# Optimization experiments

Hardware: AMD Instinct MI355X
Metric: run time of the kernel (lower is better)

## Reference

```python
import jax, jax.numpy as jnp
import numpy as np

ND, NP_, NC, H, L, B = 4000, 19000, 1000, 128, 2, 30000
E_DP, E_PP, E_CP = 200000, 300000, 150000


def setup_inputs() -> dict:
    key = jax.random.key(0)
    ks = iter(jax.random.split(key, 64))
    def nrm(shape, s=0.05):
        return jax.random.normal(next(ks), shape, dtype=jnp.float32) * s
    inp = {
        'drug_emb': nrm((ND, H)), 'protein_emb': nrm((NP_, H)), 'cell_emb': nrm((NC, H)),
    }
    for r in ['dp', 'rdp', 'pp', 'cp', 'rcp']:
        inp['W_' + r] = nrm((L, H, H))
        inp['a_src_' + r] = nrm((L, H))
        inp['a_dst_' + r] = nrm((L, H))
        inp['b_' + r] = jnp.zeros((L, H), jnp.float32)
    inp['W1'] = nrm((3 * H, 6 * H)); inp['b1'] = jnp.zeros((6 * H,), jnp.float32)
    inp['W2'] = nrm((6 * H, 2 * H)); inp['b2'] = jnp.zeros((2 * H,), jnp.float32)
    inp['W3'] = nrm((2 * H, 2)); inp['b3'] = jnp.zeros((2,), jnp.float32)
    def ri(n, hi):
        return jax.random.randint(next(ks), (n,), 0, hi, dtype=jnp.int32)
    inp['src_dp'] = ri(E_DP, ND); inp['dst_dp'] = ri(E_DP, NP_)
    inp['src_pp'] = ri(E_PP, NP_); inp['dst_pp'] = ri(E_PP, NP_)
    inp['src_cp'] = ri(E_CP, NC); inp['dst_cp'] = ri(E_CP, NP_)
    inp['drug1'] = ri(B, ND); inp['drug2'] = ri(B, ND); inp['cell'] = ri(B, NC)
    return inp


def _gat(x_src, x_dst, W, a_s, a_d, b, src, dst, n_dst):
    # Single-head PyG GATConv: shared linear, additive attention, segment softmax over dst.
    h_s = x_src @ W                      # [Ns, H]
    h_d = x_dst @ W                      # [Nd, H]
    e = jax.nn.leaky_relu((h_s @ a_s)[src] + (h_d @ a_d)[dst], 0.2)  # [E]
    m = jax.lax.stop_gradient(jax.ops.segment_max(e, dst, num_segments=n_dst))
    p = jnp.exp(e - m[dst])
    denom = jax.ops.segment_sum(p, dst, num_segments=n_dst)
    alpha = p / denom[dst]
    out = jax.ops.segment_sum(alpha[:, None] * h_s[src], dst, num_segments=n_dst)
    return out + b


def _l2norm(x):
    return x / jnp.maximum(jnp.linalg.norm(x, axis=1, keepdims=True), 1e-12)


def reference(drug_emb, protein_emb, cell_emb,
              W_dp, a_src_dp, a_dst_dp, b_dp,
              W_rdp, a_src_rdp, a_dst_rdp, b_rdp,
              W_pp, a_src_pp, a_dst_pp, b_pp,
              W_cp, a_src_cp, a_dst_cp, b_cp,
              W_rcp, a_src_rcp, a_dst_rcp, b_rcp,
              W1, b1, W2, b2, W3, b3,
              src_dp, dst_dp, src_pp, dst_pp, src_cp, dst_cp,
              drug1, drug2, cell):
    # p-p uses add_self_loops=True
    loops = jnp.arange(NP_, dtype=src_pp.dtype)
    spp = jnp.concatenate([src_pp, loops]); dpp = jnp.concatenate([dst_pp, loops])
    x_d, x_p, x_c = drug_emb, protein_emb, cell_emb
    for l in range(L):
        out_p = _gat(x_d, x_p, W_dp[l], a_src_dp[l], a_dst_dp[l], b_dp[l], src_dp, dst_dp, NP_)
        out_p = out_p + _gat(x_p, x_p, W_pp[l], a_src_pp[l], a_dst_pp[l], b_pp[l], spp, dpp, NP_)
        out_p = out_p + _gat(x_c, x_p, W_cp[l], a_src_cp[l], a_dst_cp[l], b_cp[l], src_cp, dst_cp, NP_)
        out_d = _gat(x_p, x_d, W_rdp[l], a_src_rdp[l], a_dst_rdp[l], b_rdp[l], dst_dp, src_dp, ND)
        out_c = _gat(x_p, x_c, W_rcp[l], a_src_rcp[l], a_dst_rcp[l], b_rcp[l], dst_cp, src_cp, NC)
        x_d, x_p, x_c = jax.nn.relu(out_d), jax.nn.relu(out_p), jax.nn.relu(out_c)
    hid = jnp.concatenate([_l2norm(x_d[drug1]), _l2norm(x_d[drug2]), _l2norm(x_c[cell])], axis=1)
    h = jax.nn.relu(hid @ W1 + b1)
    h = jax.nn.relu(h @ W2 + b2)
    return h @ W3 + b3
```

## Files before the change

### kernel.cpp

```cpp
#include <hip/hip_runtime.h>
#include <hip/hip_bf16.h>

#define H 128
#define ND 4000
#define NPN 19000
#define NCN 1000
#define NLAYERS 2
#define NB 30000
#define E_DP 200000
#define E_PP 300000
#define E_CP 150000

typedef __bf16 bf16_t;
typedef bf16_t bf16x8 __attribute__((ext_vector_type(8)));
typedef float f32x4 __attribute__((ext_vector_type(4)));
typedef unsigned short u16;

static __device__ __forceinline__ float wred_sum(float v) {
#pragma unroll
  for (int off = 32; off; off >>= 1) v += __shfl_xor(v, off);
  return v;
}
static __device__ __forceinline__ float bflo(unsigned u) { return __uint_as_float(u << 16); }
static __device__ __forceinline__ float bfhi(unsigned u) { return __uint_as_float(u & 0xffff0000u); }
static __device__ __forceinline__ unsigned packbf(float v0, float v1) {
  union { bf16_t b; unsigned short u; } a, b;
  a.b = (bf16_t)v0; b.b = (bf16_t)v1;
  return (unsigned)a.u | ((unsigned)b.u << 16);
}

#define GLDS16(gp, lp) \
  __builtin_amdgcn_global_load_lds((__attribute__((address_space(1))) void*)(gp), \
                                   (__attribute__((address_space(3))) void*)(lp), 16, 0, 0)

__device__ __forceinline__ void mfma_core(
    const bf16_t* __restrict__ A, const bf16_t* __restrict__ Bt,
    int M, int K, int ldb, int m0, int n0, f32x4 (&acc)[4][4])
{
  __shared__ char As[128 * 64];
  __shared__ char Bs[128 * 64];
  const int t = threadIdx.x;
  const int lane = t & 63;
#pragma unroll
  for (int mi = 0; mi < 4; ++mi)
#pragma unroll
    for (int ni = 0; ni < 4; ++ni) acc[mi][ni] = (f32x4){0.f, 0.f, 0.f, 0.f};

  const int wid = t >> 6;
  const int wr = wid >> 1, wc = wid & 1;
  const int sr = t >> 2;
  const int sc = t & 3;
  const int csrc = ((sc ^ ((sr >> 1) & 3)) << 4);
  int ra0 = m0 + sr;      if (ra0 >= M) ra0 = M - 1;
  int ra1 = m0 + 64 + sr; if (ra1 >= M) ra1 = M - 1;
  const char* gA0 = (const char*)A + (size_t)ra0 * K * 2 + csrc;
  const char* gA1 = (const char*)A + (size_t)ra1 * K * 2 + csrc;
  const char* gB0 = (const char*)Bt + (size_t)(n0 + sr) * ldb * 2 + csrc;
  const char* gB1 = (const char*)Bt + (size_t)(n0 + 64 + sr) * ldb * 2 + csrc;
  char* lA0 = As + t * 16;
  char* lA1 = As + 4096 + t * 16;
  char* lB0 = Bs + t * 16;
  char* lB1 = Bs + 4096 + t * 16;

  int aoff[4], boff[4];
#pragma unroll
  for (int mi = 0; mi < 4; ++mi) {
    int r = wr * 64 + mi * 16 + (lane & 15);
    aoff[mi] = r * 64 + ((((lane >> 4)) ^ ((r >> 1) & 3)) << 4);
  }
#pragma unroll
  for (int ni = 0; ni < 4; ++ni) {
    int r = wc * 64 + ni * 16 + (lane & 15);
    boff[ni] = r * 64 + ((((lane >> 4)) ^ ((r >> 1) & 3)) << 4);
  }

  for (int k0 = 0; k0 < K; k0 += 32) {
    const size_t kb = (size_t)k0 * 2;
    __syncthreads();
    GLDS16(gA0 + kb, lA0);
    GLDS16(gA1 + kb, lA1);
    GLDS16(gB0 + kb, lB0);
    GLDS16(gB1 + kb, lB1);
    __syncthreads();
    bf16x8 av[4], bv[4];
#pragma unroll
    for (int mi = 0; mi < 4; ++mi) av[mi] = *(const bf16x8*)(As + aoff[mi]);
#pragma unroll
    for (int ni = 0; ni < 4; ++ni) bv[ni] = *(const bf16x8*)(Bs + boff[ni]);
#pragma unroll
    for (int mi = 0; mi < 4; ++mi)
#pragma unroll
      for (int ni = 0; ni < 4; ++ni)
        acc[mi][ni] = __builtin_amdgcn_mfma_f32_16x16x32_bf16(av[mi], bv[ni], acc[mi][ni], 0, 0, 0);
  }
}

struct GJob { const bf16_t* A; const bf16_t* Bt; bf16_t* C; int M; int K;
              const float *b1, *b2, *b3; };
struct Gemm3 { GJob j[3]; };
__global__ __launch_bounds__(256) void k_gemm_g3(Gemm3 g) {
  const GJob& jb = g.j[blockIdx.y];
  int m0 = blockIdx.x * 128;
  if (m0 >= jb.M) return;
  f32x4 acc[4][4];
  mfma_core(jb.A, jb.Bt, jb.M, jb.K, jb.K, m0, 0, acc);
  const int t = threadIdx.x, lane = t & 63, wid = t >> 6;
  const int wr = wid >> 1, wc = wid & 1;
  const int col0 = lane & 15, rsub = (lane >> 4) * 4;
#pragma unroll
  for (int mi = 0; mi < 4; ++mi) {
#pragma unroll
    for (int ni = 0; ni < 4; ++ni) {
      int c = wc * 64 + ni * 16 + col0;
      float bb = jb.b1[c];
      if (jb.b2) bb += jb.b2[c];
      if (jb.b3) bb += jb.b3[c];
#pragma unroll
      for (int rg = 0; rg < 4; ++rg) {
        int r = m0 + wr * 64 + mi * 16 + rsub + rg;
        if (r < jb.M) jb.C[(size_t)r * H + c] = (bf16_t)fmaxf(acc[mi][ni][rg] + bb, 0.f);
      }
    }
  }
}

struct PJob { const bf16_t* A; float* C; int M; const float* rs; };
struct GemmPS { PJob j[3]; const bf16_t* Bt; };
__global__ __launch_bounds__(256) void k_gemm_ps(GemmPS g) {
  const PJob& jb = g.j[blockIdx.y];
  int mt = blockIdx.x / 6, nt = blockIdx.x - mt * 6;
  int m0 = mt * 128;
  if (m0 >= jb.M) return;
  int n0 = nt * 128;
  f32x4 acc[4][4];
  mfma_core(jb.A, g.Bt + blockIdx.y * 128, jb.M, 128, 384, m0, n0, acc);
  const int t = threadIdx.x, lane = t & 63, wid = t >> 6;
  const int wr = wid >> 1, wc = wid & 1;
  const int col0 = lane & 15, rsub = (lane >> 4) * 4;
#pragma unroll
  for (int mi = 0; mi < 4; ++mi) {
#pragma unroll
    for (int rg = 0; rg < 4; ++rg) {
      int r = m0 + wr * 64 + mi * 16 + rsub + rg;
      if (r < jb.M) {
        float sc = jb.rs[r];
#pragma unroll
        for (int ni = 0; ni < 4; ++ni) {
          int c = n0 + wc * 64 + ni * 16 + col0;
          jb.C[(size_t)r * 768 + c] = acc[mi][ni][rg] * sc;
        }
      }
    }
  }
}

__global__ __launch_bounds__(256) void k_w2head(
    const float* __restrict__ Pa, const float* __restrict__ Pb, const float* __restrict__ Pc,
    const float* __restrict__ b1,
    const int* __restrict__ d1, const int* __restrict__ d2, const int* __restrict__ ce,
    const bf16_t* __restrict__ W2t, const float* __restrict__ b2,
    const float* __restrict__ W3, const float* __restrict__ b3,
    float* __restrict__ out, int cn)
{
  __shared__ char As[128 * 64];
  __shared__ char Bs[128 * 64];
  const int t = threadIdx.x;
  const int lane = t & 63;
  const int m0 = blockIdx.x * 128;
  const int n0 = blockIdx.y * 128;
  if (m0 >= cn) return;
  f32x4 acc[4][4];
#pragma unroll
  for (int mi = 0; mi < 4; ++mi)
#pragma unroll
    for (int ni = 0; ni < 4; ++ni) acc[mi][ni] = (f32x4){0.f, 0.f, 0.f, 0.f};

  const int arow = t >> 1;
  const int ah = t & 1;
  int gr = m0 + arow; if (gr >= cn) gr = cn - 1;
  const float* pa = Pa + (size_t)d1[gr] * 768 + ah * 16;
  const float* pb = Pb + (size_t)d2[gr] * 768 + ah * 16;
  const float* pc = Pc + (size_t)ce[gr] * 768 + ah * 16;
  const int swz = (arow >> 1) & 3;
  char* la0 = As + arow * 64 + (((ah * 2)     ^ swz) << 4);
  char* la1 = As + arow * 64 + (((ah * 2 + 1) ^ swz) << 4);

  const int sr = t >> 2;
  const int sc = t & 3;
  const int csrc = ((sc ^ ((sr >> 1) & 3)) << 4);
  const char* gB0 = (const char*)W2t + (size_t)(n0 + sr) * 768 * 2 + csrc;
  const char* gB1 = (const char*)W2t + (size_t)(n0 + 64 + sr) * 768 * 2 + csrc;
  char* lB0 = Bs + t * 16;
  char* lB1 = Bs + 4096 + t * 16;

  const int wid = t >> 6;
  const int wr = wid >> 1, wc = wid & 1;
  int aoff[4], boff[4];
#pragma unroll
  for (int mi = 0; mi < 4; ++mi) {
    int r = wr * 64 + mi * 16 + (lane & 15);
    aoff[mi] = r * 64 + ((((lane >> 4)) ^ ((r >> 1) & 3)) << 4);
  }
#pragma unroll
  for (int ni = 0; ni < 4; ++ni) {
    int r = wc * 64 + ni * 16 + (lane & 15);
    boff[ni] = r * 64 + ((((lane >> 4)) ^ ((r >> 1) & 3)) << 4);
  }

  for (int k0 = 0; k0 < 768; k0 += 32) {
    const float4* qa = (const float4*)(pa + k0);
    const float4* qb = (const float4*)(pb + k0);
    const float4* qc = (const float4*)(pc + k0);
    const float4* qb1 = (const float4*)(b1 + k0 + ah * 16);
    float4 A0 = qa[0], A1 = qa[1], A2 = qa[2], A3 = qa[3];
    float4 B0 = qb[0], B1 = qb[1], B2 = qb[2], B3 = qb[3];
    float4 C0 = qc[0], C1 = qc[1], C2 = qc[2], C3 = qc[3];
    float4 D0 = qb1[0], D1 = qb1[1], D2 = qb1[2], D3 = qb1[3];
    uint4 P0, P1;
    P0.x = packbf(fmaxf(A0.x + B0.x + C0.x + D0.x, 0.f), fmaxf(A0.y + B0.y + C0.y + D0.y, 0.f));
    P0.y = packbf(fmaxf(A0.z + B0.z + C0.z + D0.z, 0.f), fmaxf(A0.w + B0.w + C0.w + D0.w, 0.f));
    P0.z = packbf(fmaxf(A1.x + B1.x + C1.x + D1.x, 0.f), fmaxf(A1.y + B1.y + C1.y + D1.y, 0.f));
    P0.w = packbf(fmaxf(A1.z + B1.z + C1.z + D1.z, 0.f), fmaxf(A1.w + B1.w + C1.w + D1.w, 0.f));
    P1.x = packbf(fmaxf(A2.x + B2.x + C2.x + D2.x, 0.f), fmaxf(A2.y + B2.y + C2.y + D2.y, 0.f));
    P1.y = packbf(fmaxf(A2.z + B2.z + C2.z + D2.z, 0.f), fmaxf(A2.w + B2.w + C2.w + D2.w, 0.f));
    P1.z = packbf(fmaxf(A3.x + B3.x + C3.x + D3.x, 0.f), fmaxf(A3.y + B3.y + C3.y + D3.y, 0.f));
    P1.w = packbf(fmaxf(A3.z + B3.z + C3.z + D3.z, 0.f), fmaxf(A3.w + B3.w + C3.w + D3.w, 0.f));
    __syncthreads();
    GLDS16(gB0 + (size_t)k0 * 2, lB0);
    GLDS16(gB1 + (size_t)k0 * 2, lB1);
    *(uint4*)la0 = P0;
    *(uint4*)la1 = P1;
    __syncthreads();
    bf16x8 av[4], bv[4];
#pragma unroll
    for (int mi = 0; mi < 4; ++mi) av[mi] = *(const bf16x8*)(As + aoff[mi]);
#pragma unroll
    for (int ni = 0; ni < 4; ++ni) bv[ni] = *(const bf16x8*)(Bs + boff[ni]);
#pragma unroll
    for (int mi = 0; mi < 4; ++mi)
#pragma unroll
      for (int ni = 0; ni < 4; ++ni)
        acc[mi][ni] = __builtin_amdgcn_mfma_f32_16x16x32_bf16(av[mi], bv[ni], acc[mi][ni], 0, 0, 0);
  }

  const int col0 = lane & 15, rsub = (lane >> 4) * 4;
  float w0[4], w1[4], bb[4];
#pragma unroll
  for (int ni = 0; ni < 4; ++ni) {
    int c = n0 + wc * 64 + ni * 16 + col0;
    w0[ni] = W3[2 * c]; w1[ni] = W3[2 * c + 1]; bb[ni] = b2[c];
  }
  const int addb = (n0 == 0 && wc == 0);
#pragma unroll
  for (int mi = 0; mi < 4; ++mi) {
#pragma unroll
    for (int rg = 0; rg < 4; ++rg) {
      int r = m0 + wr * 64 + mi * 16 + rsub + rg;
      float p0 = 0.f, p1 = 0.f;
#pragma unroll
      for (int ni = 0; ni < 4; ++ni) {
        float v = fmaxf(acc[mi][ni][rg] + bb[ni], 0.f);
        p0 = fmaf(v, w0[ni], p0);
        p1 = fmaf(v, w1[ni], p1);
      }
#pragma unroll
      for (int off = 1; off < 16; off <<= 1) {
        p0 += __shfl_xor(p0, off);
        p1 += __shfl_xor(p1, off);
      }
      if (col0 == 0 && r < cn) {
        if (addb) { p0 += b3[0]; p1 += b3[1]; }
        atomicAdd(&out[(size_t)r * 2], p0);
        atomicAdd(&out[(size_t)r * 2 + 1], p1);
      }
    }
  }
}

__global__ __launch_bounds__(256) void k_conv_emb(
    const float* __restrict__ xd, const float* __restrict__ xp, const float* __restrict__ xc,
    bf16_t* __restrict__ od, bf16_t* __restrict__ op, bf16_t* __restrict__ oc)
{
  int i = blockIdx.x * 256 + threadIdx.x;
  const int SD = ND * H, SP = NPN * H, SC = NCN * H;
  if (i < SD) od[i] = (bf16_t)xd[i];
  else if (i < SD + SP) op[i - SD] = (bf16_t)xp[i - SD];
  else if (i < SD + SP + SC) oc[i - SD - SP] = (bf16_t)xc[i - SD - SP];
}

struct TC { const float* src[12]; bf16_t* dst[12]; int Ksub[12]; int N[12]; int Kfull[12]; int koff[12]; };
__global__ __launch_bounds__(256) void k_tconv2(TC a) {
  int m = blockIdx.z;
  int Ks = a.Ksub[m], N = a.N[m];
  int tx = blockIdx.x * 32;
  int ty = blockIdx.y * 32;
  if (tx >= N || ty >= Ks) return;
  __shared__ float tile[32][33];
  int c = threadIdx.x & 31, rr = threadIdx.x >> 5;
#pragma unroll
  for (int kk = rr; kk < 32; kk += 8)
    if (ty + kk < Ks && tx + c < N) tile[kk][c] = a.src[m][(size_t)(ty + kk) * N + tx + c];
  __syncthreads();
  bf16_t* dst = a.dst[m];
  int Kf = a.Kfull[m], ko = a.koff[m];
#pragma unroll
  for (int nn = rr; nn < 32; nn += 8)
    if (tx + nn < N && ty + c < Ks)
      dst[(size_t)(tx + nn) * Kf + ko + ty + c] = (bf16_t)tile[c][nn];
}

struct Wd20 { const float* W[20]; const float* a[20]; float* o[20]; };
__global__ __launch_bounds__(128) void k_wd20(Wd20 g) {
  int m = blockIdx.x;
  int k = threadIdx.x;
  const float* Wp = g.W[m];
  const float* av = g.a[m];
  float s = 0.f;
#pragma unroll 4
  for (int j = 0; j < H; ++j) s = fmaf(Wp[k * H + j], av[j], s);
  g.o[m][k] = s;
}

struct Sc { const bf16_t* xd; const bf16_t* xp; const bf16_t* xc; const float* wv;
            float* ss[5]; float* sd[5]; };
__global__ __launch_bounds__(256) void k_scores(Sc S) {
  int row = blockIdx.x * 4 + (threadIdx.x >> 6);
  if (row >= ND + NPN + NCN) return;
  int lane = threadIdx.x & 63;
  const bf16_t* x;
  int idx, cls;
  if (row < ND) { x = S.xd; idx = row; cls = 0; }
  else if (row < ND + NPN) { x = S.xp; idx = row - ND; cls = 1; }
  else { x = S.xc; idx = row - ND - NPN; cls = 2; }
  unsigned u = *(const unsigned*)(x + (size_t)idx * H + lane * 2);
  float x0 = bflo(u), x1 = bfhi(u);
  const float* wv = S.wv;
#define DOT(vi, outp) { const float* v = wv + (vi) * H; \
    float s = x0 * v[2 * lane] + x1 * v[2 * lane + 1]; s = wred_sum(s); \
    if (!lane) (outp)[idx] = s; }
  if (cls == 0) {
    DOT(0, S.ss[0]); DOT(8, S.sd[3]);
  } else if (cls == 1) {
    DOT(1, S.ss[1]); DOT(3, S.ss[3]); DOT(4, S.ss[4]);
    DOT(5, S.sd[0]); DOT(6, S.sd[1]); DOT(7, S.sd[2]);
  } else {
    DOT(2, S.ss[2]); DOT(9, S.sd[4]);
  }
#undef DOT
}

struct CsrArgs {
  const int* src[5]; const int* dst[5];
  int E[5]; int n[5];
  int* cnt[5]; int* cur[5]; int* starts[5]; u16* csr[5];
};
__global__ __launch_bounds__(256) void k_count5(CsrArgs a) {
  int rel = blockIdx.y;
  int E = a.E[rel];
  const int* dst = a.dst[rel];
  int* cnt = a.cnt[rel];
  int e0 = blockIdx.x * 1024 + threadIdx.x;
#pragma unroll
  for (int u = 0; u < 4; ++u) {
    int e = e0 + u * 256;
    if (e < E) atomicAdd(&cnt[dst[e]], 1);
  }
}
__global__ __launch_bounds__(1024) void k_scan5(CsrArgs a) {
  int rel = blockIdx.x;
  int n = a.n[rel];
  const int* cnt = a.cnt[rel];
  int* st = a.starts[rel];
  int* cu = a.cur[rel];
  int t = threadIdx.x;
  int stripe = (n + 1023) / 1024;
  int lo = t * stripe;
  int hi = lo + stripe; if (hi > n) hi = n;
  int s = 0;
  for (int i = lo; i < hi; ++i) s += cnt[i];
  int lane = t & 63, wv = t >> 6;
  int x = s;
#pragma unroll
  for (int off = 1; off < 64; off <<= 1) {
    int y = __shfl_up(x, off);
    if (lane >= off) x += y;
  }
  __shared__ int ws[16];
  if (lane == 63) ws[wv] = x;
  __syncthreads();
  if (t == 0) {
    int run = 0;
#pragma unroll
    for (int i = 0; i < 16; ++i) { int v = ws[i]; ws[i] = run; run += v; }
  }
  __syncthreads();
  int run = ws[wv] + x - s;
  for (int i = lo; i < hi; ++i) { st[i] = run; cu[i] = run; run += cnt[i]; }
  if (t == 1023) st[n] = ws[15] + x;
}
__global__ __launch_bounds__(256) void k_fill5(CsrArgs a) {
  int rel = blockIdx.y;
  int E = a.E[rel];
  const int* dst = a.dst[rel];
  const int* src = a.src[rel];
  int* cur = a.cur[rel];
  u16* csr = a.csr[rel];
  int e0 = blockIdx.x * 1024 + threadIdx.x;
#pragma unroll
  for (int u = 0; u < 4; ++u) {
    int e = e0 + u * 256;
    if (e < E) {
      int pos = atomicAdd(&cur[dst[e]], 1);
      csr[pos] = (u16)src[e];
    }
  }
}

struct Agg5 {
  const u16* csr[5]; const int* starts[5];
  const float* ss[5]; const float* sd[5];
  const bf16_t* xs[5];
  bf16_t* y[5]; int ystride[5]; int ycoff[5]; int ndst[5]; int self[5];
};
__global__ __launch_bounds__(256) void k_agg5(Agg5 a) {
  int rel = blockIdx.y;
  int d = blockIdx.x * 4 + (threadIdx.x >> 6);
  if (d >= a.ndst[rel]) return;
  int lane = threadIdx.x & 63;
  int g = lane >> 4, j16 = lane & 15;
  bf16_t* yrow = a.y[rel] + (size_t)d * a.ystride[rel] + a.ycoff[rel];
  int s0 = a.starts[rel][d];
  int deg = a.starts[rel][d + 1] - s0;
  int selfa = a.self[rel];
  if (!deg && !selfa) {
    if (g == 0) *(uint4*)(yrow + j16 * 8) = make_uint4(0u, 0u, 0u, 0u);
    return;
  }
  const u16* cs = a.csr[rel] + s0;
  const float* ssp = a.ss[rel];
  const bf16_t* xsp = a.xs[rel];
  float sdv = a.sd[rel][d];
  float acc[8] = {0.f, 0.f, 0.f, 0.f, 0.f, 0.f, 0.f, 0.f};
  float ps = 0.f;
  for (int b = 0; b < deg; b += 16) {
#pragma unroll
    for (int u = 0; u < 4; ++u) {
      int i = b + u * 4 + g;
      float p = 0.f;
      uint4 U = make_uint4(0u, 0u, 0u, 0u);
      if (i < deg) {
        int s = cs[i];
        float e = ssp[s] + sdv; e = e > 0.f ? e : 0.2f * e;
        p = __expf(e);
        U = *(const uint4*)(xsp + (size_t)s * H + j16 * 8);
      }
      ps += p;
      acc[0] = fmaf(p, bflo(U.x), acc[0]); acc[1] = fmaf(p, bfhi(U.x), acc[1]);
      acc[2] = fmaf(p, bflo(U.y), acc[2]); acc[3] = fmaf(p, bfhi(U.y), acc[3]);
      acc[4] = fmaf(p, bflo(U.z), acc[4]); acc[5] = fmaf(p, bfhi(U.z), acc[5]);
      acc[6] = fmaf(p, bflo(U.w), acc[6]); acc[7] = fmaf(p, bfhi(U.w), acc[7]);
    }
  }
  if (selfa && g == 0) {
    float e = ssp[d] + sdv; e = e > 0.f ? e : 0.2f * e;
    float p = __expf(e);
    uint4 U = *(const uint4*)(xsp + (size_t)d * H + j16 * 8);
    ps += p;
    acc[0] = fmaf(p, bflo(U.x), acc[0]); acc[1] = fmaf(p, bfhi(U.x), acc[1]);
    acc[2] = fmaf(p, bflo(U.y), acc[2]); acc[3] = fmaf(p, bfhi(U.y), acc[3]);
    acc[4] = fmaf(p, bflo(U.z), acc[4]); acc[5] = fmaf(p, bfhi(U.z), acc[5]);
    acc[6] = fmaf(p, bflo(U.w), acc[6]); acc[7] = fmaf(p, bfhi(U.w), acc[7]);
  }
#pragma unroll
  for (int e = 0; e < 8; ++e) {
    acc[e] += __shfl_xor(acc[e], 16);
    acc[e] += __shfl_xor(acc[e], 32);
  }
  ps += __shfl_xor(ps, 16);
  ps += __shfl_xor(ps, 32);
  if (g == 0) {
    float inv = 1.f / ps;
    uint4 O;
    O.x = packbf(acc[0] * inv, acc[1] * inv);
    O.y = packbf(acc[2] * inv, acc[3] * inv);
    O.z = packbf(acc[4] * inv, acc[5] * inv);
    O.w = packbf(acc[6] * inv, acc[7] * inv);
    *(uint4*)(yrow + j16 * 8) = O;
  }
}

__global__ __launch_bounds__(256) void k_invnorm(
    const bf16_t* __restrict__ xd, const bf16_t* __restrict__ xc,
    float* __restrict__ invd, float* __restrict__ invc)
{
  int row = blockIdx.x * 4 + (threadIdx.x >> 6);
  if (row >= ND + NCN) return;
  int lane = threadIdx.x & 63;
  const bf16_t* x = (row < ND) ? xd + (size_t)row * H : xc + (size_t)(row - ND) * H;
  unsigned u = ((const unsigned*)x)[lane];
  float av = bflo(u), bv = bfhi(u);
  float s = wred_sum(av * av + bv * bv);
  if (!lane) {
    float nv = fmaxf(sqrtf(s), 1e-12f);
    if (row < ND) invd[row] = 1.f / nv; else invc[row - ND] = 1.f / nv;
  }
}

extern "C" void kernel_launch(void* const* d_in, const int* in_sizes, int n_in,
                              void* d_out, int out_size, void* d_ws, size_t ws_size,
                              hipStream_t stream)
{
  (void)in_sizes; (void)n_in;
  const float* drug_emb    = (const float*)d_in[0];
  const float* protein_emb = (const float*)d_in[1];
  const float* cell_emb    = (const float*)d_in[2];
  const int base_idx[5] = {3, 11, 15, 7, 19};
  const float *W_[5], *as_[5], *ad_[5], *b_[5];
  for (int r = 0; r < 5; ++r) {
    W_[r]  = (const float*)d_in[base_idx[r]];
    as_[r] = (const float*)d_in[base_idx[r] + 1];
    ad_[r] = (const float*)d_in[base_idx[r] + 2];
    b_[r]  = (const float*)d_in[base_idx[r] + 3];
  }
  const float* W1 = (const float*)d_in[23]; const float* b1 = (const float*)d_in[24];
  const float* W2 = (const float*)d_in[25]; const float* b2 = (const float*)d_in[26];
  const float* W3 = (const float*)d_in[27]; const float* b3 = (const float*)d_in[28];
  const int* src_dp = (const int*)d_in[29]; const int* dst_dp = (const int*)d_in[30];
  const int* src_pp = (const int*)d_in[31]; const int* dst_pp = (const int*)d_in[32];
  const int* src_cp = (const int*)d_in[33]; const int* dst_cp = (const int*)d_in[34];
  const int* drug1  = (const int*)d_in[35]; const int* drug2  = (const int*)d_in[36];
  const int* cellb  = (const int*)d_in[37];
  float* out = (float*)d_out;

  char* wsb = (char*)d_ws;
  size_t off = 0;
  auto alloc = [&](size_t bytes) -> void* {
    void* p = wsb + off;
    off += (bytes + 255) & ~(size_t)255;
    return p;
  };
  bf16_t* xdb[2] = {(bf16_t*)alloc((size_t)ND * H * 2),  (bf16_t*)alloc((size_t)ND * H * 2)};
  bf16_t* xpb[2] = {(bf16_t*)alloc((size_t)NPN * H * 2), (bf16_t*)alloc((size_t)NPN * H * 2)};
  bf16_t* xcb[2] = {(bf16_t*)alloc((size_t)NCN * H * 2), (bf16_t*)alloc((size_t)NCN * H * 2)};
  const int Msrc[5] = {ND, NPN, NCN, NPN, NPN};
  const int Mdst[5] = {NPN, NPN, NPN, ND, NCN};
  const int Erel[5] = {E_DP, E_PP, E_CP, E_DP, E_CP};
  bf16_t* yp = (bf16_t*)alloc((size_t)NPN * 384 * 2);
  bf16_t* yd = (bf16_t*)alloc((size_t)ND * H * 2);
  bf16_t* yc = (bf16_t*)alloc((size_t)NCN * H * 2);
  bf16_t* Wtp = (bf16_t*)alloc((size_t)NLAYERS * 128 * 384 * 2);
  bf16_t* Wtd = (bf16_t*)alloc((size_t)NLAYERS * 128 * 128 * 2);
  bf16_t* Wtc = (bf16_t*)alloc((size_t)NLAYERS * 128 * 128 * 2);
  bf16_t* W1t = (bf16_t*)alloc((size_t)768 * 384 * 2);
  bf16_t* W2t = (bf16_t*)alloc((size_t)256 * 768 * 2);
  float* wvb = (float*)alloc(20 * H * 4);
  float* ssb[5]; for (int r = 0; r < 5; ++r) ssb[r] = (float*)alloc((size_t)Msrc[r] * 4);
  float* sdb[5]; for (int r = 0; r < 5; ++r) sdb[r] = (float*)alloc((size_t)Mdst[r] * 4);
  int* cnt_all = (int*)alloc(62000 * 4);
  int* cur_all = (int*)alloc(62000 * 4);
  int* st_all  = (int*)alloc((62000 + 5) * 4);
  int *cntb[5], *curb[5], *stb[5];
  { int o = 0, o2 = 0;
    for (int r = 0; r < 5; ++r) {
      cntb[r] = cnt_all + o; curb[r] = cur_all + o; stb[r] = st_all + o2;
      o += Mdst[r]; o2 += Mdst[r] + 1;
    } }
  u16* csrb[5]; for (int r = 0; r < 5; ++r) csrb[r] = (u16*)alloc((size_t)Erel[r] * 2);
  float* invd = (float*)alloc(ND * 4);
  float* invc = (float*)alloc(NCN * 4);
  float* P1a = (float*)alloc((size_t)ND * 768 * 4);
  float* P1b = (float*)alloc((size_t)ND * 768 * 4);
  float* P1c = (float*)alloc((size_t)NCN * 768 * 4);
  (void)ws_size;

  hipMemsetAsync(out, 0, (size_t)out_size * 4, stream);

  k_conv_emb<<<(ND * H + NPN * H + NCN * H + 255) / 256, 256, 0, stream>>>(
      drug_emb, protein_emb, cell_emb, xdb[0], xpb[0], xcb[0]);
  TC tc;
  for (int l = 0; l < 2; ++l) {
    for (int r = 0; r < 3; ++r) {
      int m = l * 3 + r;
      tc.src[m] = W_[r] + (size_t)l * H * H;
      tc.dst[m] = Wtp + (size_t)l * 128 * 384;
      tc.Ksub[m] = 128; tc.N[m] = 128; tc.Kfull[m] = 384; tc.koff[m] = r * 128;
    }
    tc.src[6 + l] = W_[3] + (size_t)l * H * H; tc.dst[6 + l] = Wtd + (size_t)l * 128 * 128;
    tc.Ksub[6 + l] = 128; tc.N[6 + l] = 128; tc.Kfull[6 + l] = 128; tc.koff[6 + l] = 0;
    tc.src[8 + l] = W_[4] + (size_t)l * H * H; tc.dst[8 + l] = Wtc + (size_t)l * 128 * 128;
    tc.Ksub[8 + l] = 128; tc.N[8 + l] = 128; tc.Kfull[8 + l] = 128; tc.koff[8 + l] = 0;
  }
  tc.src[10] = W1; tc.dst[10] = W1t; tc.Ksub[10] = 384; tc.N[10] = 768; tc.Kfull[10] = 384; tc.koff[10] = 0;
  tc.src[11] = W2; tc.dst[11] = W2t; tc.Ksub[11] = 768; tc.N[11] = 256; tc.Kfull[11] = 768; tc.koff[11] = 0;
  k_tconv2<<<dim3(24, 24, 12), 256, 0, stream>>>(tc);

  Wd20 wg;
  for (int l = 0; l < 2; ++l)
    for (int r = 0; r < 5; ++r) {
      int m = l * 10 + r;
      wg.W[m] = W_[r] + (size_t)l * H * H; wg.a[m] = as_[r] + l * H; wg.o[m] = wvb + m * H;
      int m2 = l * 10 + 5 + r;
      wg.W[m2] = W_[r] + (size_t)l * H * H; wg.a[m2] = ad_[r] + l * H; wg.o[m2] = wvb + m2 * H;
    }
  k_wd20<<<20, 128, 0, stream>>>(wg);

  hipMemsetAsync(cnt_all, 0, 62000 * 4, stream);
  CsrArgs ca;
  const int* srcA[5] = {src_dp, src_pp, src_cp, dst_dp, dst_cp};
  const int* dstA[5] = {dst_dp, dst_pp, dst_cp, src_dp, src_cp};
  for (int r = 0; r < 5; ++r) {
    ca.src[r] = srcA[r]; ca.dst[r] = dstA[r]; ca.E[r] = Erel[r]; ca.n[r] = Mdst[r];
    ca.cnt[r] = cntb[r]; ca.cur[r] = curb[r]; ca.starts[r] = stb[r]; ca.csr[r] = csrb[r];
  }
  dim3 egrid((E_PP + 1023) / 1024, 5);
  k_count5<<<egrid, 256, 0, stream>>>(ca);
  k_scan5<<<5, 1024, 0, stream>>>(ca);
  k_fill5<<<egrid, 256, 0, stream>>>(ca);

  int cur = 0;
  for (int l = 0; l < NLAYERS; ++l) {
    int nxt = 1 - cur;
    const bf16_t* xsrc[5] = {xdb[cur], xpb[cur], xcb[cur], xpb[cur], xpb[cur]};
    Sc sc;
    sc.xd = xdb[cur]; sc.xp = xpb[cur]; sc.xc = xcb[cur]; sc.wv = wvb + l * 10 * H;
    for (int r = 0; r < 5; ++r) { sc.ss[r] = ssb[r]; sc.sd[r] = sdb[r]; }
    k_scores<<<(ND + NPN + NCN + 3) / 4, 256, 0, stream>>>(sc);
    Agg5 aa;
    bf16_t* yptr[5] = {yp, yp, yp, yd, yc};
    const int ystr[5] = {384, 384, 384, 128, 128};
    const int ycof[5] = {0, 128, 256, 0, 0};
    const int selfs[5] = {0, 1, 0, 0, 0};
    for (int r = 0; r < 5; ++r) {
      aa.csr[r] = csrb[r]; aa.starts[r] = stb[r]; aa.ss[r] = ssb[r]; aa.sd[r] = sdb[r];
      aa.xs[r] = xsrc[r]; aa.y[r] = yptr[r]; aa.ystride[r] = ystr[r]; aa.ycoff[r] = ycof[r];
      aa.ndst[r] = Mdst[r]; aa.self[r] = selfs[r];
    }
    k_agg5<<<dim3((NPN + 3) / 4, 5), 256, 0, stream>>>(aa);
    Gemm3 g3;
    g3.j[0] = {yp, Wtp + (size_t)l * 128 * 384, xpb[nxt], NPN, 384,
               b_[0] + l * H, b_[1] + l * H, b_[2] + l * H};
    g3.j[1] = {yd, Wtd + (size_t)l * 128 * 128, xdb[nxt], ND, 128,
               b_[3] + l * H, nullptr, nullptr};
    g3.j[2] = {yc, Wtc + (size_t)l * 128 * 128, xcb[nxt], NCN, 128,
               b_[4] + l * H, nullptr, nullptr};
    k_gemm_g3<<<dim3((NPN + 127) / 128, 3), 256, 0, stream>>>(g3);
    cur = nxt;
  }

  k_invnorm<<<(ND + NCN + 3) / 4, 256, 0, stream>>>(xdb[cur], xcb[cur], invd, invc);
  GemmPS ps;
  ps.Bt = W1t;
  ps.j[0] = {xdb[cur], P1a, ND, invd};
  ps.j[1] = {xdb[cur], P1b, ND, invd};
  ps.j[2] = {xcb[cur], P1c, NCN, invc};
  k_gemm_ps<<<dim3(32 * 6, 3), 256, 0, stream>>>(ps);
  k_w2head<<<dim3((NB + 127) / 128, 2), 256, 0, stream>>>(
      P1a, P1b, P1c, b1, drug1, drug2, cellb, W2t, b2, W3, b3, out, NB);
}
```

Before: 418.3 us.

## Store W1 partial products in bf16, fold bias, widen head tile to full N

The per-table W1 partial products now go to bf16 instead of fp32, with a third of b1 folded into each partial so the head kernel no longer reads b1. The head kernel now covers all 256 output columns in one block instead of splitting N over two blocks. This halves the gathered bytes and avoids gathering each row twice. In exchange it doubles accumulator registers per thread, which may lower occupancy, and adds extra bf16 rounding in the partial sums.

```diff
diff --git a/kernel.cpp b/kernel.cpp
--- a/kernel.cpp
+++ b/kernel.cpp
@@ -124,8 +124,8 @@
   }
 }
 
-struct PJob { const bf16_t* A; float* C; int M; const float* rs; };
-struct GemmPS { PJob j[3]; const bf16_t* Bt; };
+struct PJob { const bf16_t* A; bf16_t* C; int M; const float* rs; };
+struct GemmPS { PJob j[3]; const bf16_t* Bt; const float* b1t; };
 __global__ __launch_bounds__(256) void k_gemm_ps(GemmPS g) {
   const PJob& jb = g.j[blockIdx.y];
   int mt = blockIdx.x / 6, nt = blockIdx.x - mt * 6;
@@ -147,7 +147,7 @@
 #pragma unroll
         for (int ni = 0; ni < 4; ++ni) {
           int c = n0 + wc * 64 + ni * 16 + col0;
-          jb.C[(size_t)r * 768 + c] = acc[mi][ni][rg] * sc;
+          jb.C[(size_t)r * 768 + c] = (bf16_t)(acc[mi][ni][rg] * sc + g.b1t[c]);
         }
       }
     }
@@ -155,32 +155,30 @@
 }
 
 __global__ __launch_bounds__(256) void k_w2head(
-    const float* __restrict__ Pa, const float* __restrict__ Pb, const float* __restrict__ Pc,
-    const float* __restrict__ b1,
+    const bf16_t* __restrict__ Pa, const bf16_t* __restrict__ Pb, const bf16_t* __restrict__ Pc,
     const int* __restrict__ d1, const int* __restrict__ d2, const int* __restrict__ ce,
     const bf16_t* __restrict__ W2t, const float* __restrict__ b2,
     const float* __restrict__ W3, const float* __restrict__ b3,
     float* __restrict__ out, int cn)
 {
   __shared__ char As[128 * 64];
-  __shared__ char Bs[128 * 64];
+  __shared__ char Bs[256 * 64];
   const int t = threadIdx.x;
   const int lane = t & 63;
   const int m0 = blockIdx.x * 128;
-  const int n0 = blockIdx.y * 128;
   if (m0 >= cn) return;
-  f32x4 acc[4][4];
+  f32x4 acc[4][8];
 #pragma unroll
   for (int mi = 0; mi < 4; ++mi)
 #pragma unroll
-    for (int ni = 0; ni < 4; ++ni) acc[mi][ni] = (f32x4){0.f, 0.f, 0.f, 0.f};
+    for (int ni = 0; ni < 8; ++ni) acc[mi][ni] = (f32x4){0.f, 0.f, 0.f, 0.f};
 
   const int arow = t >> 1;
   const int ah = t & 1;
   int gr = m0 + arow; if (gr >= cn) gr = cn - 1;
-  const float* pa = Pa + (size_t)d1[gr] * 768 + ah * 16;
-  const float* pb = Pb + (size_t)d2[gr] * 768 + ah * 16;
-  const float* pc = Pc + (size_t)ce[gr] * 768 + ah * 16;
+  const bf16_t* pa = Pa + (size_t)d1[gr] * 768 + ah * 16;
+  const bf16_t* pb = Pb + (size_t)d2[gr] * 768 + ah * 16;
+  const bf16_t* pc = Pc + (size_t)ce[gr] * 768 + ah * 16;
   const int swz = (arow >> 1) & 3;
   char* la0 = As + arow * 64 + (((ah * 2)     ^ swz) << 4);
   char* la1 = As + arow * 64 + (((ah * 2 + 1) ^ swz) << 4);
@@ -188,69 +186,75 @@
   const int sr = t >> 2;
   const int sc = t & 3;
   const int csrc = ((sc ^ ((sr >> 1) & 3)) << 4);
-  const char* gB0 = (const char*)W2t + (size_t)(n0 + sr) * 768 * 2 + csrc;
-  const char* gB1 = (const char*)W2t + (size_t)(n0 + 64 + sr) * 768 * 2 + csrc;
-  char* lB0 = Bs + t * 16;
-  char* lB1 = Bs + 4096 + t * 16;
+  const char* gB = (const char*)W2t + (size_t)sr * 768 * 2 + csrc;
+  const size_t qstep = (size_t)64 * 768 * 2;
 
   const int wid = t >> 6;
   const int wr = wid >> 1, wc = wid & 1;
-  int aoff[4], boff[4];
+  int aoff[4], boff[8];
 #pragma unroll
   for (int mi = 0; mi < 4; ++mi) {
     int r = wr * 64 + mi * 16 + (lane & 15);
     aoff[mi] = r * 64 + ((((lane >> 4)) ^ ((r >> 1) & 3)) << 4);
   }
 #pragma unroll
-  for (int ni = 0; ni < 4; ++ni) {
-    int r = wc * 64 + ni * 16 + (lane & 15);
+  for (int ni = 0; ni < 8; ++ni) {
+    int r = wc * 128 + ni * 16 + (lane & 15);
     boff[ni] = r * 64 + ((((lane >> 4)) ^ ((r >> 1) & 3)) << 4);
   }
 
+#define ACC8(U, o) { s[o+0] += bflo(U.x); s[o+1] += bfhi(U.x); s[o+2] += bflo(U.y); s[o+3] += bfhi(U.y); \
+                     s[o+4] += bflo(U.z); s[o+5] += bfhi(U.z); s[o+6] += bflo(U.w); s[o+7] += bfhi(U.w); }
   for (int k0 = 0; k0 < 768; k0 += 32) {
-    const float4* qa = (const float4*)(pa + k0);
-    const float4* qb = (const float4*)(pb + k0);
-    const float4* qc = (const float4*)(pc + k0);
-    const float4* qb1 = (const float4*)(b1 + k0 + ah * 16);
-    float4 A0 = qa[0], A1 = qa[1], A2 = qa[2], A3 = qa[3];
-    float4 B0 = qb[0], B1 = qb[1], B2 = qb[2], B3 = qb[3];
-    float4 C0 = qc[0], C1 = qc[1], C2 = qc[2], C3 = qc[3];
-    float4 D0 = qb1[0], D1 = qb1[1], D2 = qb1[2], D3 = qb1[3];
+    uint4 Ua0 = *(const uint4*)(pa + k0);
+    uint4 Ua1 = *(const uint4*)(pa + k0 + 8);
+    uint4 Ub0 = *(const uint4*)(pb + k0);
+    uint4 Ub1 = *(const uint4*)(pb + k0 + 8);
+    uint4 Uc0 = *(const uint4*)(pc + k0);
+    uint4 Uc1 = *(const uint4*)(pc + k0 + 8);
+    float s[16] = {0.f, 0.f, 0.f, 0.f, 0.f, 0.f, 0.f, 0.f,
+                   0.f, 0.f, 0.f, 0.f, 0.f, 0.f, 0.f, 0.f};
+    ACC8(Ua0, 0) ACC8(Ua1, 8)
+    ACC8(Ub0, 0) ACC8(Ub1, 8)
+    ACC8(Uc0, 0) ACC8(Uc1, 8)
     uint4 P0, P1;
-    P0.x = packbf(fmaxf(A0.x + B0.x + C0.x + D0.x, 0.f), fmaxf(A0.y + B0.y + C0.y + D0.y, 0.f));
-    P0.y = packbf(fmaxf(A0.z + B0.z + C0.z + D0.z, 0.f), fmaxf(A0.w + B0.w + C0.w + D0.w, 0.f));
-    P0.z = packbf(fmaxf(A1.x + B1.x + C1.x + D1.x, 0.f), fmaxf(A1.y + B1.y + C1.y + D1.y, 0.f));
-    P0.w = packbf(fmaxf(A1.z + B1.z + C1.z + D1.z, 0.f), fmaxf(A1.w + B1.w + C1.w + D1.w, 0.f));
-    P1.x = packbf(fmaxf(A2.x + B2.x + C2.x + D2.x, 0.f), fmaxf(A2.y + B2.y + C2.y + D2.y, 0.f));
-    P1.y = packbf(fmaxf(A2.z + B2.z + C2.z + D2.z, 0.f), fmaxf(A2.w + B2.w + C2.w + D2.w, 0.f));
-    P1.z = packbf(fmaxf(A3.x + B3.x + C3.x + D3.x, 0.f), fmaxf(A3.y + B3.y + C3.y + D3.y, 0.f));
-    P1.w = packbf(fmaxf(A3.z + B3.z + C3.z + D3.z, 0.f), fmaxf(A3.w + B3.w + C3.w + D3.w, 0.f));
+    P0.x = packbf(fmaxf(s[0], 0.f),  fmaxf(s[1], 0.f));
+    P0.y = packbf(fmaxf(s[2], 0.f),  fmaxf(s[3], 0.f));
+    P0.z = packbf(fmaxf(s[4], 0.f),  fmaxf(s[5], 0.f));
+    P0.w = packbf(fmaxf(s[6], 0.f),  fmaxf(s[7], 0.f));
+    P1.x = packbf(fmaxf(s[8], 0.f),  fmaxf(s[9], 0.f));
+    P1.y = packbf(fmaxf(s[10], 0.f), fmaxf(s[11], 0.f));
+    P1.z = packbf(fmaxf(s[12], 0.f), fmaxf(s[13], 0.f));
+    P1.w = packbf(fmaxf(s[14], 0.f), fmaxf(s[15], 0.f));
+    const size_t kb = (size_t)k0 * 2;
     __syncthreads();
-    GLDS16(gB0 + (size_t)k0 * 2, lB0);
-    GLDS16(gB1 + (size_t)k0 * 2, lB1);
+    GLDS16(gB + kb,             Bs + t * 16);
+    GLDS16(gB + qstep + kb,     Bs + 4096 + t * 16);
+    GLDS16(gB + 2 * qstep + kb, Bs + 8192 + t * 16);
+    GLDS16(gB + 3 * qstep + kb, Bs + 12288 + t * 16);
     *(uint4*)la0 = P0;
     *(uint4*)la1 = P1;
     __syncthreads();
-    bf16x8 av[4], bv[4];
+    bf16x8 av[4], bv[8];
 #pragma unroll
     for (int mi = 0; mi < 4; ++mi) av[mi] = *(const bf16x8*)(As + aoff[mi]);
 #pragma unroll
-    for (int ni = 0; ni < 4; ++ni) bv[ni] = *(const bf16x8*)(Bs + boff[ni]);
+    for (int ni = 0; ni < 8; ++ni) bv[ni] = *(const bf16x8*)(Bs + boff[ni]);
 #pragma unroll
     for (int mi = 0; mi < 4; ++mi)
 #pragma unroll
-      for (int ni = 0; ni < 4; ++ni)
+      for (int ni = 0; ni < 8; ++ni)
         acc[mi][ni] = __builtin_amdgcn_mfma_f32_16x16x32_bf16(av[mi], bv[ni], acc[mi][ni], 0, 0, 0);
   }
+#undef ACC8
 
   const int col0 = lane & 15, rsub = (lane >> 4) * 4;
-  float w0[4], w1[4], bb[4];
-#pragma unroll
-  for (int ni = 0; ni < 4; ++ni) {
-    int c = n0 + wc * 64 + ni * 16 + col0;
+  float w0[8], w1[8], bb[8];
+#pragma unroll
+  for (int ni = 0; ni < 8; ++ni) {
+    int c = wc * 128 + ni * 16 + col0;
     w0[ni] = W3[2 * c]; w1[ni] = W3[2 * c + 1]; bb[ni] = b2[c];
   }
-  const int addb = (n0 == 0 && wc == 0);
 #pragma unroll
   for (int mi = 0; mi < 4; ++mi) {
 #pragma unroll
@@ -258,7 +262,7 @@
       int r = m0 + wr * 64 + mi * 16 + rsub + rg;
       float p0 = 0.f, p1 = 0.f;
 #pragma unroll
-      for (int ni = 0; ni < 4; ++ni) {
+      for (int ni = 0; ni < 8; ++ni) {
         float v = fmaxf(acc[mi][ni][rg] + bb[ni], 0.f);
         p0 = fmaf(v, w0[ni], p0);
         p1 = fmaf(v, w1[ni], p1);
@@ -269,7 +273,7 @@
         p1 += __shfl_xor(p1, off);
       }
       if (col0 == 0 && r < cn) {
-        if (addb) { p0 += b3[0]; p1 += b3[1]; }
+        if (wc == 0) { p0 += b3[0]; p1 += b3[1]; }
         atomicAdd(&out[(size_t)r * 2], p0);
         atomicAdd(&out[(size_t)r * 2 + 1], p1);
       }
@@ -286,6 +290,11 @@
   if (i < SD) od[i] = (bf16_t)xd[i];
   else if (i < SD + SP) op[i - SD] = (bf16_t)xp[i - SD];
   else if (i < SD + SP + SC) oc[i - SD - SP] = (bf16_t)xc[i - SD - SP];
+}
+
+__global__ __launch_bounds__(256) void k_scale3(const float* __restrict__ b1, float* __restrict__ o) {
+  int i = blockIdx.x * 256 + threadIdx.x;
+  if (i < 768) o[i] = b1[i] * (1.f / 3.f);
 }
 
 struct TC { const float* src[12]; bf16_t* dst[12]; int Ksub[12]; int N[12]; int Kfull[12]; int koff[12]; };
@@ -554,6 +563,7 @@
   bf16_t* W1t = (bf16_t*)alloc((size_t)768 * 384 * 2);
   bf16_t* W2t = (bf16_t*)alloc((size_t)256 * 768 * 2);
   float* wvb = (float*)alloc(20 * H * 4);
+  float* b1t = (float*)alloc(768 * 4);
   float* ssb[5]; for (int r = 0; r < 5; ++r) ssb[r] = (float*)alloc((size_t)Msrc[r] * 4);
   float* sdb[5]; for (int r = 0; r < 5; ++r) sdb[r] = (float*)alloc((size_t)Mdst[r] * 4);
   int* cnt_all = (int*)alloc(62000 * 4);
@@ -568,15 +578,16 @@
   u16* csrb[5]; for (int r = 0; r < 5; ++r) csrb[r] = (u16*)alloc((size_t)Erel[r] * 2);
   float* invd = (float*)alloc(ND * 4);
   float* invc = (float*)alloc(NCN * 4);
-  float* P1a = (float*)alloc((size_t)ND * 768 * 4);
-  float* P1b = (float*)alloc((size_t)ND * 768 * 4);
-  float* P1c = (float*)alloc((size_t)NCN * 768 * 4);
+  bf16_t* P1a = (bf16_t*)alloc((size_t)ND * 768 * 2);
+  bf16_t* P1b = (bf16_t*)alloc((size_t)ND * 768 * 2);
+  bf16_t* P1c = (bf16_t*)alloc((size_t)NCN * 768 * 2);
   (void)ws_size;
 
   hipMemsetAsync(out, 0, (size_t)out_size * 4, stream);
 
   k_conv_emb<<<(ND * H + NPN * H + NCN * H + 255) / 256, 256, 0, stream>>>(
       drug_emb, protein_emb, cell_emb, xdb[0], xpb[0], xcb[0]);
+  k_scale3<<<3, 256, 0, stream>>>(b1, b1t);
   TC tc;
   for (int l = 0; l < 2; ++l) {
     for (int r = 0; r < 3; ++r) {
@@ -649,11 +660,11 @@
 
   k_invnorm<<<(ND + NCN + 3) / 4, 256, 0, stream>>>(xdb[cur], xcb[cur], invd, invc);
   GemmPS ps;
-  ps.Bt = W1t;
+  ps.Bt = W1t; ps.b1t = b1t;
   ps.j[0] = {xdb[cur], P1a, ND, invd};
   ps.j[1] = {xdb[cur], P1b, ND, invd};
   ps.j[2] = {xcb[cur], P1c, NCN, invc};
   k_gemm_ps<<<dim3(32 * 6, 3), 256, 0, stream>>>(ps);
-  k_w2head<<<dim3((NB + 127) / 128, 2), 256, 0, stream>>>(
-      P1a, P1b, P1c, b1, drug1, drug2, cellb, W2t, b2, W3, b3, out, NB);
-}
+  k_w2head<<<(NB + 127) / 128, 256, 0, stream>>>(
+      P1a, P1b, P1c, drug1, drug2, cellb, W2t, b2, W3, b3, out, NB);
+}
```

Measured after the change: 400.6 us. 4.2% less time.
